# Kernel tuning notes

Hardware: AMD Instinct MI355X
Metric: run time of the kernel (lower is better)

The kernel has to match this reference:

```python
import jax, jax.numpy as jnp
import numpy as np

EPS = 1e-6      # VN nonlinearity eps
BN_EPS = 1e-5   # torch BatchNorm default eps


def setup_inputs() -> dict:
    key = jax.random.key(0)
    k1, k2, k3 = jax.random.split(key, 3)
    B, Cin, N = 8, 64, 2048
    Cout = 64
    x = jax.random.normal(k1, (B, Cin, 3, N), dtype=jnp.float32)
    # nn.Linear(in, out, bias=False) weights: [out, in], kaiming-uniform-ish scale
    s = 1.0 / np.sqrt(Cin)
    W_feat = jax.random.uniform(k2, (Cout, Cin), jnp.float32, -s, s)
    W_dir = jax.random.uniform(k3, (Cout, Cin), jnp.float32, -s, s)
    gamma = jnp.ones((Cout,), jnp.float32)
    beta = jnp.zeros((Cout,), jnp.float32)
    return {"x": x, "W_feat": W_feat, "W_dir": W_dir, "gamma": gamma, "beta": beta, "k": 10}


def _knn_idx(xf, kk):
    # xf: [B, D, N]; returns indices of kk nearest neighbors (incl. self), [B, N, kk]
    xx = jnp.sum(xf * xf, axis=1)                       # [B, N]
    inner = jnp.einsum('bdn,bdm->bnm', xf, xf)          # [B, N, N]
    pdist = 2.0 * inner - xx[:, :, None] - xx[:, None, :]  # = -||xi-xj||^2
    _, idx = jax.lax.top_k(pdist, kk)                   # largest = nearest
    return idx


def reference(x, W_feat, W_dir, gamma, beta, k):
    B, Cin, _, N = x.shape
    K = k + 1
    xf = x.reshape(B, Cin * 3, N)                       # [B, 3*Cin, N]
    idx = _knn_idx(xf, K)                               # [B, N, K]

    # gather neighbor features: [B, N, K, 3*Cin]
    xT = jnp.transpose(xf, (0, 2, 1))                   # [B, N, 3*Cin]
    feat = jax.vmap(lambda xt, id_: xt[id_])(xT, idx)   # [B, N, K, 3*Cin]
    feat = feat.reshape(B, N, K, Cin, 3)
    feat = jnp.transpose(feat, (0, 3, 4, 1, 2))         # [B, Cin, 3, N, K]

    # VN linear
    p = jnp.einsum('oc,bcdnk->bodnk', W_feat, feat)     # [B, Cout, 3, N, K]

    # VNBatchNorm (training-mode batch stats, biased var) on vector norms
    norm = jnp.sqrt(jnp.sum(p * p, axis=2))             # [B, Cout, N, K]
    mean = jnp.mean(norm, axis=(0, 2, 3))
    var = jnp.var(norm, axis=(0, 2, 3))
    norm_bn = (norm - mean[None, :, None, None]) * jax.lax.rsqrt(var + BN_EPS)[None, :, None, None]
    norm_bn = norm_bn * gamma[None, :, None, None] + beta[None, :, None, None]
    p = p / norm[:, :, None] * norm_bn[:, :, None]

    # direction + conditional vector nonlinearity
    d = jnp.einsum('oc,bcdnk->bodnk', W_dir, feat)      # [B, Cout, 3, N, K]
    dot = jnp.sum(p * d, axis=2, keepdims=True)         # [B, Cout, 1, N, K]
    d_sq = jnp.sum(d * d, axis=2, keepdims=True)
    x_out = jnp.where(dot >= 0, p, p - dot / (d_sq + EPS) * d)

    return jnp.mean(x_out, axis=-1)                     # [B, Cout, 3, N]
```

## Files before the change

kernel.cpp:

```cpp
#include <hip/hip_runtime.h>
#include <stdint.h>

#define B_   8
#define D_   192
#define N_   2048
#define KNb  11

using u32 = uint32_t;
using u16 = unsigned short;
typedef _Float16 f16;
struct alignas(8) h4 { f16 x, y, z, w; };

typedef __attribute__((ext_vector_type(8)))  short short8;
typedef __attribute__((ext_vector_type(16))) float f32x16;

__device__ __forceinline__ float bf2f(u16 h){ union{u32 i; float f;} x; x.i = ((u32)h) << 16; return x.f; }
__device__ __forceinline__ u16 f2bf(float f){
  union{float f; u32 i;} x; x.f = f;
  u32 r = (x.i + 0x7fffu + ((x.i >> 16) & 1u)) >> 16;
  return (u16)r;
}
__device__ __forceinline__ u32 umax32(u32 a, u32 b){ return a > b ? a : b; }
__device__ __forceinline__ u32 umin32(u32 a, u32 b){ return a < b ? a : b; }

__global__ __launch_bounds__(256) void split_kernel(const float* __restrict__ x,
                                                    short* __restrict__ Xs,
                                                    float* __restrict__ xT,
                                                    double* __restrict__ xxd){
  __shared__ float A[D_ * 64];
  const int b = blockIdx.y, m0 = blockIdx.x * 64, t = threadIdx.x;
  const size_t xb = (size_t)b * D_ * N_;
  #pragma unroll
  for (int q = 0; q < 48; ++q){
    int p = t + 256*q;
    int d = p >> 6, i = p & 63;
    A[d*64 + i] = x[xb + (size_t)d*N_ + m0 + i];
  }
  __syncthreads();

  {
    const int l = t & 63, wv = t >> 6;
    const int lh = l >> 5, l31 = l & 31;
    #pragma unroll
    for (int j = 0; j < 6; ++j){
      int p  = j*4 + wv;
      int tt = p / 12, c = p % 12;
      int dbase = c*16 + lh*8;
      int row = tt*32 + l31;
      union{ u16 s[8]; int4 v; } u;
      #pragma unroll
      for (int q = 0; q < 8; ++q) u.s[q] = f2bf(A[(dbase + q)*64 + row]);
      size_t P = ((size_t)b*64 + blockIdx.x*2 + tt)*12 + c;
      *(int4*)(Xs + P*512 + l*8) = u.v;
    }
  }
  {
    const int m = t & 63, seg = t >> 6;
    float* trow = xT + ((size_t)b*N_ + m0 + m) * 192 + seg*48;
    #pragma unroll
    for (int j = 0; j < 12; ++j){
      float4 v = { A[(seg*48 + 4*j + 0)*64 + m], A[(seg*48 + 4*j + 1)*64 + m],
                   A[(seg*48 + 4*j + 2)*64 + m], A[(seg*48 + 4*j + 3)*64 + m] };
      *(float4*)(trow + 4*j) = v;
    }
  }
  if (t < 64){
    double s = 0.0;
    #pragma unroll 4
    for (int d = 0; d < D_; ++d){ double v = (double)A[d*64 + t]; s = fma(v, v, s); }
    xxd[b*N_ + m0 + t] = s;
  }
}

#define KLA   0
#define KLCT  12288
#define KLXXS 45568
#define KLXXN 46592
#define KLSZ  46720
__global__ __launch_bounds__(512, 6) void knn_kernel(const short* __restrict__ Xs,
                                                     const double* __restrict__ xxd,
                                                     u16* __restrict__ cand){
  __shared__ __align__(16) char smem[KLSZ];
  float* CT  = (float*)(smem + KLCT);
  float* XXS = (float*)(smem + KLXXS);
  float* XXN = (float*)(smem + KLXXN);

  const int b = blockIdx.x, n0 = blockIdx.y * 32;
  const int t = threadIdx.x, lane = t & 63, w = t >> 6;
  const int l31 = lane & 31, lh = lane >> 5;

  {
    const short* Ap = Xs + (((size_t)b*64 + (n0 >> 5)) * 12) * 512;
    #pragma unroll
    for (int j = 0; j < 2; ++j){
      int p = t + 512*j;
      if (j == 0 || t < 256){
        int4 v = *(const int4*)(Ap + (size_t)p*8);
        *(int4*)(smem + KLA + p*16) = v;
      }
    }
  }
  if (t < 32) XXN[t] = (float)xxd[b*N_ + n0 + t];

  u32 key[10];
  #pragma unroll
  for (int j = 0; j < 10; ++j) key[j] = 0u;

  for (int st = 0; st < 8; ++st){
    const int m0 = st * 256;
    __syncthreads();
    if (t < 256) XXS[t] = (float)xxd[b*N_ + m0 + t];

    const short* Bp = Xs + (((size_t)b*64 + (m0 >> 5) + w) * 12) * 512 + lane*8;
    short8 b0 = *(const short8*)(Bp + 0*512);
    short8 b1 = *(const short8*)(Bp + 1*512);
    short8 c0 = *(const short8*)(Bp + 2*512);
    short8 c1 = *(const short8*)(Bp + 3*512);
    short8 d0 = *(const short8*)(Bp + 4*512);
    short8 d1 = *(const short8*)(Bp + 5*512);
    f32x16 acc = (f32x16)0.0f;
    #pragma unroll
    for (int kc = 0; kc < 6; ++kc){
      short8 a0 = *(const short8*)(smem + KLA + (kc*2+0)*1024 + lane*16);
      short8 a1 = *(const short8*)(smem + KLA + (kc*2+1)*1024 + lane*16);
      acc = __builtin_amdgcn_mfma_f32_32x32x16_bf16(a0, b0, acc, 0, 0, 0);
      acc = __builtin_amdgcn_mfma_f32_32x32x16_bf16(a1, b1, acc, 0, 0, 0);
      b0 = c0; b1 = c1; c0 = d0; c1 = d1;
      if (kc < 3){
        d0 = *(const short8*)(Bp + (kc*2+6)*512);
        d1 = *(const short8*)(Bp + (kc*2+7)*512);
      }
    }

    #pragma unroll
    for (int reg = 0; reg < 16; ++reg){
      int r = (reg & 3) + 8*(reg >> 2) + 4*lh;
      CT[r*260 + w*32 + l31] = acc[reg];
    }
    __syncthreads();

    {
      const int r = t & 31, sub = t >> 5;
      const float xn = XXN[r];
      const float* ctp = CT + r*260 + sub*16;
      const float* xsp = XXS + sub*16;
      const int mb = m0 + sub*16;
      #pragma unroll
      for (int q = 0; q < 4; ++q){
        float4 cv = *(const float4*)(ctp + 4*q);
        float4 xv = *(const float4*)(xsp + 4*q);
        float vs[4]  = {cv.x, cv.y, cv.z, cv.w};
        float xs4[4] = {xv.x, xv.y, xv.z, xv.w};
        #pragma unroll
        for (int j = 0; j < 4; ++j){
          float v = fmaf(2.f, vs[j], -(xs4[j] + xn));
          u32 bbits = __float_as_uint(v);
          u32 kk = ((bbits ^ (u32)(((int)bbits >> 31) | 0x80000000)) & 0xFFFFF800u)
                   | (u32)(mb + 4*q + j);
          #pragma unroll
          for (int s = 0; s < 9; ++s) key[s] = umin32(key[s+1], umax32(kk, key[s]));
          key[9] = umax32(kk, key[9]);
        }
      }
    }
  }

  __syncthreads();
  u32* MVK = (u32*)(smem + KLCT);
  {
    const int r = t & 31, sub = t >> 5;
    #pragma unroll
    for (int j = 0; j < 10; ++j) MVK[(sub*32 + r)*10 + j] = key[j];
  }
  __syncthreads();
  if (t < 32){
    int head[16];
    #pragma unroll
    for (int q = 0; q < 16; ++q) head[q] = 9;
    const size_t ob = ((size_t)b*N_ + n0 + t) * 16;
    for (int s = 0; s < 16; ++s){
      u32 best = 0u; int bq = 0;
      #pragma unroll
      for (int q = 0; q < 16; ++q){
        int hh = head[q];
        u32 v = (hh >= 0) ? MVK[(q*32 + t)*10 + hh] : 0u;
        if (v > best){ best = v; bq = q; }
      }
      cand[ob + s] = (u16)(best & 2047u);
      #pragma unroll
      for (int q = 0; q < 16; ++q) head[q] -= (q == bq) ? 1 : 0;
    }
  }
}

__global__ __launch_bounds__(256) void refine_kernel(const float* __restrict__ xT,
                                                     const u16* __restrict__ cand,
                                                     const double* __restrict__ xxd,
                                                     int* __restrict__ idxout){
  const int wv = threadIdx.x >> 6, ln = threadIdx.x & 63;
  const int g = blockIdx.x * 4 + wv;
  const int b = g >> 11, n = g & 2047;
  const int c = ln >> 2, part = ln & 3;
  const int m = (int)cand[(size_t)g*16 + c] & 2047;
  const float4* pn = (const float4*)(xT + ((size_t)b*N_ + n)*192 + part*48);
  const float4* pm = (const float4*)(xT + ((size_t)b*N_ + m)*192 + part*48);
  double s = 0.0;
  #pragma unroll
  for (int j = 0; j < 12; ++j){
    float4 a = pn[j], bb = pm[j];
    s = fma((double)a.x, (double)bb.x, s);
    s = fma((double)a.y, (double)bb.y, s);
    s = fma((double)a.z, (double)bb.z, s);
    s = fma((double)a.w, (double)bb.w, s);
  }
  s += __shfl_down(s, 2, 64);
  s += __shfl_down(s, 1, 64);
  double v = 2.0*s - xxd[b*N_ + n] - xxd[b*N_ + m];
  int rank = 0;
  #pragma unroll
  for (int q = 0; q < 16; ++q){
    double vq = __shfl(v, q*4, 64);
    int    mq = __shfl(m, q*4, 64);
    bool beat = (vq > v) || ((vq == v) && (mq < m));
    rank += beat ? 1 : 0;
  }
  if (part == 0 && rank < KNb)
    idxout[(size_t)g*KNb + rank] = m;
}

__global__ __launch_bounds__(256) void project_kernel(const float* __restrict__ xT,
                                                      const float* __restrict__ Wf,
                                                      const float* __restrict__ Wd,
                                                      h4* __restrict__ P0h,
                                                      h4* __restrict__ D0h){
  __shared__ float A[16 * 192];
  const int b = blockIdx.x, m0 = blockIdx.y * 16, t = threadIdx.x;
  const int c = t & 63, mg = t >> 6;

  float wf[64], wd[64];
  #pragma unroll
  for (int q = 0; q < 16; ++q){
    float4 uf = *(const float4*)(Wf + c*64 + q*4);
    wf[q*4+0]=uf.x; wf[q*4+1]=uf.y; wf[q*4+2]=uf.z; wf[q*4+3]=uf.w;
    float4 ud = *(const float4*)(Wd + c*64 + q*4);
    wd[q*4+0]=ud.x; wd[q*4+1]=ud.y; wd[q*4+2]=ud.z; wd[q*4+3]=ud.w;
  }
  {
    const float4* src = (const float4*)(xT + ((size_t)b*N_ + m0)*192);
    float4* dst = (float4*)A;
    #pragma unroll
    for (int j = 0; j < 3; ++j) dst[t + 256*j] = src[t + 256*j];
  }
  __syncthreads();

  for (int mi = 0; mi < 4; ++mi){
    int m = mg*4 + mi;
    const float4* row = (const float4*)(A + m*192);
    float p[3] = {0.f,0.f,0.f}, qv[3] = {0.f,0.f,0.f};
    #pragma unroll
    for (int v4 = 0; v4 < 48; ++v4){
      float4 f = row[v4];
      const int e = v4*4;
      p [(e+0)%3] = fmaf(wf[(e+0)/3], f.x, p [(e+0)%3]);
      qv[(e+0)%3] = fmaf(wd[(e+0)/3], f.x, qv[(e+0)%3]);
      p [(e+1)%3] = fmaf(wf[(e+1)/3], f.y, p [(e+1)%3]);
      qv[(e+1)%3] = fmaf(wd[(e+1)/3], f.y, qv[(e+1)%3]);
      p [(e+2)%3] = fmaf(wf[(e+2)/3], f.z, p [(e+2)%3]);
      qv[(e+2)%3] = fmaf(wd[(e+2)/3], f.z, qv[(e+2)%3]);
      p [(e+3)%3] = fmaf(wf[(e+3)/3], f.w, p [(e+3)%3]);
      qv[(e+3)%3] = fmaf(wd[(e+3)/3], f.w, qv[(e+3)%3]);
    }
    float nrm = sqrtf(p[0]*p[0] + p[1]*p[1] + p[2]*p[2]);
    float dsq = qv[0]*qv[0] + qv[1]*qv[1] + qv[2]*qv[2];
    size_t base = ((size_t)b*N_ + m0 + m)*64 + c;
    h4 vp; vp.x = (f16)p[0];  vp.y = (f16)p[1];  vp.z = (f16)p[2];  vp.w = (f16)nrm;
    h4 vd; vd.x = (f16)qv[0]; vd.y = (f16)qv[1]; vd.z = (f16)qv[2]; vd.w = (f16)dsq;
    P0h[base] = vp;
    D0h[base] = vd;
  }
}

__global__ __launch_bounds__(256) void count_kernel(const int* __restrict__ idxin, int* __restrict__ cnt){
  int i = blockIdx.x*256 + threadIdx.x;
  if (i < B_*N_*KNb){
    int b = i / (N_*KNb);
    atomicAdd(&cnt[b*N_ + (idxin[i] & 2047)], 1);
  }
}

__global__ __launch_bounds__(256) void stats_kernel(const h4* __restrict__ P0h,
                                                    const int* __restrict__ cnt,
                                                    float* __restrict__ gs){
  const int b = blockIdx.x >> 3;
  const int chunk = blockIdx.x & 7;
  const int w = threadIdx.x >> 6, c = threadIdx.x & 63;
  float s = 0.f, s2 = 0.f;
  const int mbase = chunk*256 + w*64;
  for (int i = 0; i < 64; ++i){
    int m = mbase + i;
    float wt = (float)cnt[b*N_ + m];
    float nv = (float)P0h[((size_t)b*N_ + m)*64 + c].w;
    s  = fmaf(wt, nv, s);
    s2 = fmaf(wt*nv, nv, s2);
  }
  __shared__ float red[8][64];
  red[w][c] = s; red[4+w][c] = s2;
  __syncthreads();
  if (w == 0) atomicAdd(&gs[c],    red[0][c]+red[1][c]+red[2][c]+red[3][c]);
  if (w == 1) atomicAdd(&gs[64+c], red[4][c]+red[5][c]+red[6][c]+red[7][c]);
}

__global__ __launch_bounds__(512) void out_kernel(const h4* __restrict__ P0h, const h4* __restrict__ D0h,
                                                  const int* __restrict__ idxin, const float* __restrict__ gs,
                                                  const float* __restrict__ gamma, const float* __restrict__ beta,
                                                  float* __restrict__ outp){
  __shared__ float res[16 * 193];
  const int b  = blockIdx.x;
  const int n0 = blockIdx.y * 16;
  const int t = threadIdx.x, w = t >> 6, c = t & 63;
  const float Ninv = 1.f / (float)(B_*N_*KNb);
  float mean = gs[c] * Ninv;
  float var  = gs[64+c] * Ninv - mean*mean;
  float istd = rsqrtf(var + 1e-5f);
  float sa = istd * gamma[c];
  float be = beta[c];
  const float kinv = 1.f/11.f;
  for (int i = 0; i < 2; ++i){
    int row = w*2 + i;
    int n = n0 + row;
    const int* ip = idxin + ((size_t)b*N_ + n)*KNb;
    float a0=0, a1=0, a2=0;
    #pragma unroll
    for (int k = 0; k < KNb; ++k){
      int m = ip[k] & 2047;
      size_t base = ((size_t)b*N_ + m)*64 + c;
      h4 P  = P0h[base];
      h4 Dv = D0h[base];
      float pw = (float)P.w;
      float nb = (pw - mean)*sa + be;
      float sc = nb / pw;
      float p0 = (float)P.x*sc, p1 = (float)P.y*sc, p2 = (float)P.z*sc;
      float d0 = (float)Dv.x, d1 = (float)Dv.y, d2 = (float)Dv.z;
      float dot = p0*d0 + p1*d1 + p2*d2;
      float f = (dot >= 0.f) ? 0.f : dot / ((float)Dv.w + 1e-6f);
      a0 += p0 - f*d0; a1 += p1 - f*d1; a2 += p2 - f*d2;
    }
    res[row*193 + 3*c + 0] = a0*kinv;
    res[row*193 + 3*c + 1] = a1*kinv;
    res[row*193 + 3*c + 2] = a2*kinv;
  }
  __syncthreads();
  {
    int p = t;
    #pragma unroll
    for (int j = 0; j < 2; ++j){
      if (p < 768){
        int cdim = p >> 2, nq = p & 3;
        float4 v = { res[(nq*4 + 0)*193 + cdim], res[(nq*4 + 1)*193 + cdim],
                     res[(nq*4 + 2)*193 + cdim], res[(nq*4 + 3)*193 + cdim] };
        *(float4*)(outp + ((size_t)b*192 + cdim)*N_ + n0 + nq*4) = v;
      }
      p += 512;
    }
  }
}

extern "C" void kernel_launch(void* const* d_in, const int* in_sizes, int n_in,
                              void* d_out, int out_size, void* d_ws, size_t ws_size,
                              hipStream_t stream){
  const float* x     = (const float*)d_in[0];
  const float* Wf    = (const float*)d_in[1];
  const float* Wd    = (const float*)d_in[2];
  const float* gamma = (const float*)d_in[3];
  const float* beta  = (const float*)d_in[4];
  float* outp = (float*)d_out;

  char* ws = (char*)d_ws;
  int*    idx  = (int*)   (ws);
  int*    cnt  = (int*)   (ws + 720896);
  float*  gs   = (float*) (ws + 786432);
  h4*     P0h  = (h4*)    (ws + 1048576);
  h4*     D0h  = (h4*)    (ws + 9437184);
  short*  Xs   = (short*) (ws + 1048576);
  double* xxd  = (double*)(ws + 13631488);
  u16*    cand = (u16*)   (ws + 13762560);
  float*  xT   = (float*) (ws + 17825792);

  hipMemsetAsync(cnt, 0, 66048, stream);
  split_kernel  <<<dim3(32, 8),  256, 0, stream>>>(x, Xs, xT, xxd);
  knn_kernel    <<<dim3(8, 64),  512, 0, stream>>>(Xs, xxd, cand);
  refine_kernel <<<4096,         256, 0, stream>>>(xT, cand, xxd, idx);
  project_kernel<<<dim3(8, 128), 256, 0, stream>>>(xT, Wf, Wd, P0h, D0h);
  count_kernel  <<<704,          256, 0, stream>>>(idx, cnt);
  stats_kernel  <<<64,           256, 0, stream>>>(P0h, cnt, gs);
  out_kernel    <<<dim3(8, 128), 512, 0, stream>>>(P0h, D0h, idx, gs, gamma, beta, outp);
}
```

Measured before the change: 257.9 us.

## Double-buffer knn key selection, fuse counting into refine, retile split and stats

Result: slower. 267.2 us (+3.6%).

```diff
diff --git a/kernel.cpp b/kernel.cpp
--- a/kernel.cpp
+++ b/kernel.cpp
@@ -14,7 +14,6 @@
 typedef __attribute__((ext_vector_type(8)))  short short8;
 typedef __attribute__((ext_vector_type(16))) float f32x16;
 
-__device__ __forceinline__ float bf2f(u16 h){ union{u32 i; float f;} x; x.i = ((u32)h) << 16; return x.f; }
 __device__ __forceinline__ u16 f2bf(float f){
   union{float f; u32 i;} x; x.f = f;
   u32 r = (x.i + 0x7fffu + ((x.i >> 16) & 1u)) >> 16;
@@ -23,18 +22,33 @@
 __device__ __forceinline__ u32 umax32(u32 a, u32 b){ return a > b ? a : b; }
 __device__ __forceinline__ u32 umin32(u32 a, u32 b){ return a < b ? a : b; }
 
+__device__ __forceinline__ void sel16(const u32* __restrict__ ctp, u32* key){
+  #pragma unroll
+  for (int q = 0; q < 4; ++q){
+    uint4 kv = *(const uint4*)(ctp + 4*q);
+    u32 ks[4] = {kv.x, kv.y, kv.z, kv.w};
+    #pragma unroll
+    for (int j = 0; j < 4; ++j){
+      u32 kk = ks[j];
+      #pragma unroll
+      for (int s = 0; s < 9; ++s) key[s] = umin32(key[s+1], umax32(kk, key[s]));
+      key[9] = umax32(kk, key[9]);
+    }
+  }
+}
+
 __global__ __launch_bounds__(256) void split_kernel(const float* __restrict__ x,
                                                     short* __restrict__ Xs,
                                                     float* __restrict__ xT,
                                                     double* __restrict__ xxd){
-  __shared__ float A[D_ * 64];
-  const int b = blockIdx.y, m0 = blockIdx.x * 64, t = threadIdx.x;
+  __shared__ float A[D_ * 32];
+  const int b = blockIdx.y, tile = blockIdx.x, m0 = tile * 32, t = threadIdx.x;
   const size_t xb = (size_t)b * D_ * N_;
   #pragma unroll
-  for (int q = 0; q < 48; ++q){
+  for (int q = 0; q < 24; ++q){
     int p = t + 256*q;
-    int d = p >> 6, i = p & 63;
-    A[d*64 + i] = x[xb + (size_t)d*N_ + m0 + i];
+    int d = p >> 5, i = p & 31;
+    A[d*32 + i] = x[xb + (size_t)d*N_ + m0 + i];
   }
   __syncthreads();
 
@@ -42,65 +56,65 @@
     const int l = t & 63, wv = t >> 6;
     const int lh = l >> 5, l31 = l & 31;
     #pragma unroll
+    for (int j = 0; j < 3; ++j){
+      int c = j*4 + wv;
+      int dbase = c*16 + lh*8;
+      union{ u16 s[8]; int4 v; } u;
+      #pragma unroll
+      for (int q = 0; q < 8; ++q) u.s[q] = f2bf(A[(dbase + q)*32 + l31]);
+      size_t P = ((size_t)b*64 + tile)*12 + c;
+      *(int4*)(Xs + P*512 + l*8) = u.v;
+    }
+  }
+  {
+    const int m = t & 31, seg = t >> 5;
+    float* trow = xT + ((size_t)b*N_ + m0 + m) * 192 + seg*24;
+    #pragma unroll
     for (int j = 0; j < 6; ++j){
-      int p  = j*4 + wv;
-      int tt = p / 12, c = p % 12;
-      int dbase = c*16 + lh*8;
-      int row = tt*32 + l31;
-      union{ u16 s[8]; int4 v; } u;
-      #pragma unroll
-      for (int q = 0; q < 8; ++q) u.s[q] = f2bf(A[(dbase + q)*64 + row]);
-      size_t P = ((size_t)b*64 + blockIdx.x*2 + tt)*12 + c;
-      *(int4*)(Xs + P*512 + l*8) = u.v;
-    }
-  }
-  {
-    const int m = t & 63, seg = t >> 6;
-    float* trow = xT + ((size_t)b*N_ + m0 + m) * 192 + seg*48;
-    #pragma unroll
-    for (int j = 0; j < 12; ++j){
-      float4 v = { A[(seg*48 + 4*j + 0)*64 + m], A[(seg*48 + 4*j + 1)*64 + m],
-                   A[(seg*48 + 4*j + 2)*64 + m], A[(seg*48 + 4*j + 3)*64 + m] };
+      float4 v = { A[(seg*24 + 4*j + 0)*32 + m], A[(seg*24 + 4*j + 1)*32 + m],
+                   A[(seg*24 + 4*j + 2)*32 + m], A[(seg*24 + 4*j + 3)*32 + m] };
       *(float4*)(trow + 4*j) = v;
     }
   }
-  if (t < 64){
+  if (t < 32){
     double s = 0.0;
     #pragma unroll 4
-    for (int d = 0; d < D_; ++d){ double v = (double)A[d*64 + t]; s = fma(v, v, s); }
+    for (int d = 0; d < D_; ++d){ double v = (double)A[d*32 + t]; s = fma(v, v, s); }
     xxd[b*N_ + m0 + t] = s;
   }
 }
 
 #define KLA   0
-#define KLCT  12288
-#define KLXXS 45568
-#define KLXXN 46592
-#define KLSZ  46720
-__global__ __launch_bounds__(512, 6) void knn_kernel(const short* __restrict__ Xs,
+#define KLCT0 12288
+#define KLCT1 45568
+#define KLSZ  78848
+__global__ __launch_bounds__(512, 4) void knn_kernel(const short* __restrict__ Xs,
                                                      const double* __restrict__ xxd,
                                                      u16* __restrict__ cand){
   __shared__ __align__(16) char smem[KLSZ];
-  float* CT  = (float*)(smem + KLCT);
-  float* XXS = (float*)(smem + KLXXS);
-  float* XXN = (float*)(smem + KLXXN);
 
   const int b = blockIdx.x, n0 = blockIdx.y * 32;
   const int t = threadIdx.x, lane = t & 63, w = t >> 6;
   const int l31 = lane & 31, lh = lane >> 5;
+  const int mcol = w*32 + l31;
 
   {
     const short* Ap = Xs + (((size_t)b*64 + (n0 >> 5)) * 12) * 512;
-    #pragma unroll
-    for (int j = 0; j < 2; ++j){
-      int p = t + 512*j;
-      if (j == 0 || t < 256){
-        int4 v = *(const int4*)(Ap + (size_t)p*8);
-        *(int4*)(smem + KLA + p*16) = v;
-      }
-    }
-  }
-  if (t < 32) XXN[t] = (float)xxd[b*N_ + n0 + t];
+    int4 v = *(const int4*)(Ap + (size_t)t*8);
+    *(int4*)(smem + KLA + t*16) = v;
+    if (t < 256){
+      int p = t + 512;
+      int4 v2 = *(const int4*)(Ap + (size_t)p*8);
+      *(int4*)(smem + KLA + p*16) = v2;
+    }
+  }
+  float xxn[16];
+  #pragma unroll
+  for (int reg = 0; reg < 16; ++reg){
+    int r = (reg & 3) + 8*(reg >> 2) + 4*lh;
+    xxn[reg] = (float)xxd[b*N_ + n0 + r];
+  }
+  __syncthreads();
 
   u32 key[10];
   #pragma unroll
@@ -108,16 +122,19 @@
 
   for (int st = 0; st < 8; ++st){
     const int m0 = st * 256;
-    __syncthreads();
-    if (t < 256) XXS[t] = (float)xxd[b*N_ + m0 + t];
-
-    const short* Bp = Xs + (((size_t)b*64 + (m0 >> 5) + w) * 12) * 512 + lane*8;
+    const short* Bp = Xs + (((size_t)b*64 + st*8 + w) * 12) * 512 + lane*8;
     short8 b0 = *(const short8*)(Bp + 0*512);
     short8 b1 = *(const short8*)(Bp + 1*512);
     short8 c0 = *(const short8*)(Bp + 2*512);
     short8 c1 = *(const short8*)(Bp + 3*512);
-    short8 d0 = *(const short8*)(Bp + 4*512);
-    short8 d1 = *(const short8*)(Bp + 5*512);
+    float xxs = (float)xxd[b*N_ + m0 + mcol];
+
+    if (st > 0){
+      const u32* ctp = (const u32*)(smem + ((st & 1) ? KLCT0 : KLCT1))
+                       + (t & 31)*260 + (t >> 5)*16;
+      sel16(ctp, key);
+    }
+
     f32x16 acc = (f32x16)0.0f;
     #pragma unroll
     for (int kc = 0; kc < 6; ++kc){
@@ -125,48 +142,33 @@
       short8 a1 = *(const short8*)(smem + KLA + (kc*2+1)*1024 + lane*16);
       acc = __builtin_amdgcn_mfma_f32_32x32x16_bf16(a0, b0, acc, 0, 0, 0);
       acc = __builtin_amdgcn_mfma_f32_32x32x16_bf16(a1, b1, acc, 0, 0, 0);
-      b0 = c0; b1 = c1; c0 = d0; c1 = d1;
-      if (kc < 3){
-        d0 = *(const short8*)(Bp + (kc*2+6)*512);
-        d1 = *(const short8*)(Bp + (kc*2+7)*512);
+      b0 = c0; b1 = c1;
+      if (kc < 4){
+        c0 = *(const short8*)(Bp + (kc*2+4)*512);
+        c1 = *(const short8*)(Bp + (kc*2+5)*512);
       }
     }
 
-    #pragma unroll
-    for (int reg = 0; reg < 16; ++reg){
-      int r = (reg & 3) + 8*(reg >> 2) + 4*lh;
-      CT[r*260 + w*32 + l31] = acc[reg];
+    {
+      u32* ctw = (u32*)(smem + ((st & 1) ? KLCT1 : KLCT0));
+      const u32 midx = (u32)(m0 + mcol);
+      #pragma unroll
+      for (int reg = 0; reg < 16; ++reg){
+        float v = fmaf(2.f, acc[reg], -(xxs + xxn[reg]));
+        u32 bb = __float_as_uint(v);
+        u32 kk = ((bb ^ (u32)(((int)bb >> 31) | 0x80000000)) & 0xFFFFF800u) | midx;
+        int r = (reg & 3) + 8*(reg >> 2) + 4*lh;
+        ctw[r*260 + mcol] = kk;
+      }
     }
     __syncthreads();
-
-    {
-      const int r = t & 31, sub = t >> 5;
-      const float xn = XXN[r];
-      const float* ctp = CT + r*260 + sub*16;
-      const float* xsp = XXS + sub*16;
-      const int mb = m0 + sub*16;
-      #pragma unroll
-      for (int q = 0; q < 4; ++q){
-        float4 cv = *(const float4*)(ctp + 4*q);
-        float4 xv = *(const float4*)(xsp + 4*q);
-        float vs[4]  = {cv.x, cv.y, cv.z, cv.w};
-        float xs4[4] = {xv.x, xv.y, xv.z, xv.w};
-        #pragma unroll
-        for (int j = 0; j < 4; ++j){
-          float v = fmaf(2.f, vs[j], -(xs4[j] + xn));
-          u32 bbits = __float_as_uint(v);
-          u32 kk = ((bbits ^ (u32)(((int)bbits >> 31) | 0x80000000)) & 0xFFFFF800u)
-                   | (u32)(mb + 4*q + j);
-          #pragma unroll
-          for (int s = 0; s < 9; ++s) key[s] = umin32(key[s+1], umax32(kk, key[s]));
-          key[9] = umax32(kk, key[9]);
-        }
-      }
-    }
-  }
-
-  __syncthreads();
-  u32* MVK = (u32*)(smem + KLCT);
+  }
+  {
+    const u32* ctp = (const u32*)(smem + KLCT1) + (t & 31)*260 + (t >> 5)*16;
+    sel16(ctp, key);
+  }
+
+  u32* MVK = (u32*)(smem + KLCT0);
   {
     const int r = t & 31, sub = t >> 5;
     #pragma unroll
@@ -196,7 +198,8 @@
 __global__ __launch_bounds__(256) void refine_kernel(const float* __restrict__ xT,
                                                      const u16* __restrict__ cand,
                                                      const double* __restrict__ xxd,
-                                                     int* __restrict__ idxout){
+                                                     int* __restrict__ idxout,
+                                                     int* __restrict__ cnt){
   const int wv = threadIdx.x >> 6, ln = threadIdx.x & 63;
   const int g = blockIdx.x * 4 + wv;
   const int b = g >> 11, n = g & 2047;
@@ -224,8 +227,10 @@
     bool beat = (vq > v) || ((vq == v) && (mq < m));
     rank += beat ? 1 : 0;
   }
-  if (part == 0 && rank < KNb)
+  if (part == 0 && rank < KNb){
     idxout[(size_t)g*KNb + rank] = m;
+    atomicAdd(&cnt[b*N_ + m], 1);
+  }
 }
 
 __global__ __launch_bounds__(256) void project_kernel(const float* __restrict__ xT,
@@ -280,23 +285,15 @@
   }
 }
 
-__global__ __launch_bounds__(256) void count_kernel(const int* __restrict__ idxin, int* __restrict__ cnt){
-  int i = blockIdx.x*256 + threadIdx.x;
-  if (i < B_*N_*KNb){
-    int b = i / (N_*KNb);
-    atomicAdd(&cnt[b*N_ + (idxin[i] & 2047)], 1);
-  }
-}
-
 __global__ __launch_bounds__(256) void stats_kernel(const h4* __restrict__ P0h,
                                                     const int* __restrict__ cnt,
                                                     float* __restrict__ gs){
-  const int b = blockIdx.x >> 3;
-  const int chunk = blockIdx.x & 7;
+  const int b = blockIdx.x >> 6;
+  const int chunk = blockIdx.x & 63;
   const int w = threadIdx.x >> 6, c = threadIdx.x & 63;
   float s = 0.f, s2 = 0.f;
-  const int mbase = chunk*256 + w*64;
-  for (int i = 0; i < 64; ++i){
+  const int mbase = chunk*32 + w*8;
+  for (int i = 0; i < 8; ++i){
     int m = mbase + i;
     float wt = (float)cnt[b*N_ + m];
     float nv = (float)P0h[((size_t)b*N_ + m)*64 + c].w;
@@ -387,11 +384,10 @@
   float*  xT   = (float*) (ws + 17825792);
 
   hipMemsetAsync(cnt, 0, 66048, stream);
-  split_kernel  <<<dim3(32, 8),  256, 0, stream>>>(x, Xs, xT, xxd);
+  split_kernel  <<<dim3(64, 8),  256, 0, stream>>>(x, Xs, xT, xxd);
   knn_kernel    <<<dim3(8, 64),  512, 0, stream>>>(Xs, xxd, cand);
-  refine_kernel <<<4096,         256, 0, stream>>>(xT, cand, xxd, idx);
+  refine_kernel <<<4096,         256, 0, stream>>>(xT, cand, xxd, idx, cnt);
   project_kernel<<<dim3(8, 128), 256, 0, stream>>>(xT, Wf, Wd, P0h, D0h);
-  count_kernel  <<<704,          256, 0, stream>>>(idx, cnt);
-  stats_kernel  <<<64,           256, 0, stream>>>(P0h, cnt, gs);
+  stats_kernel  <<<512,          256, 0, stream>>>(P0h, cnt, gs);
   out_kernel    <<<dim3(8, 128), 512, 0, stream>>>(P0h, D0h, idx, gs, gamma, beta, outp);
 }
```
